# Kernel tuning notes

Hardware: AMD Instinct MI355X
Metric: run time of the kernel (lower is better)

The kernel has to match this reference:

```python
import jax, jax.numpy as jnp
import numpy as np

D_MODEL = 512
N_HEADS = 8
KV_OPTS = (8, 4, 1)
D_K = D_MODEL // N_HEADS


def setup_inputs() -> dict:
    key = jax.random.key(0)
    ks = jax.random.split(key, 32)
    it = iter(ks)
    s = 0.02
    inp = {"x": jax.random.normal(next(it), (64, 1024, D_MODEL), dtype=jnp.float32)}
    # router params
    inp["r_w1"] = jax.random.normal(next(it), (D_MODEL, D_MODEL // 4), jnp.float32) * s
    inp["r_b1"] = jnp.zeros((D_MODEL // 4,), jnp.float32)
    inp["r_w2"] = jax.random.normal(next(it), (D_MODEL // 4, len(KV_OPTS)), jnp.float32) * s
    inp["r_b2"] = jnp.zeros((len(KV_OPTS),), jnp.float32)
    # per-expert GQA params
    for i, nkv in enumerate(KV_OPTS):
        inp[f"wq{i}"] = jax.random.normal(next(it), (D_MODEL, D_MODEL), jnp.float32) * s
        inp[f"wk{i}"] = jax.random.normal(next(it), (D_MODEL, nkv * D_K), jnp.float32) * s
        inp[f"wv{i}"] = jax.random.normal(next(it), (D_MODEL, nkv * D_K), jnp.float32) * s
        inp[f"wo{i}"] = jax.random.normal(next(it), (D_MODEL, D_MODEL), jnp.float32) * s
    return inp


def gqa(x, wq, wk, wv, wo, n_kv):
    B, S, _ = x.shape
    groups = N_HEADS // n_kv
    q = (x @ wq).reshape(B, S, N_HEADS, D_K).transpose(0, 2, 1, 3)  # [B,H,S,Dk]
    k = (x @ wk).reshape(B, S, n_kv, D_K).transpose(0, 2, 1, 3)     # [B,Kv,S,Dk]
    v = (x @ wv).reshape(B, S, n_kv, D_K).transpose(0, 2, 1, 3)
    k = jnp.repeat(k, groups, axis=1)
    v = jnp.repeat(v, groups, axis=1)
    scores = jnp.einsum('bhqd,bhkd->bhqk', q, k) / jnp.sqrt(jnp.float32(D_K))
    attn = jax.nn.softmax(scores, axis=-1)
    out = jnp.einsum('bhqk,bhkd->bhqd', attn, v)
    out = out.transpose(0, 2, 1, 3).reshape(B, S, D_MODEL)
    return out @ wo


def reference(x, r_w1, r_b1, r_w2, r_b2,
              wq0, wk0, wv0, wo0,
              wq1, wk1, wv1, wo1,
              wq2, wk2, wv2, wo2):
    routing_input = x.mean(axis=1)                      # [B, D]
    logits = jax.nn.relu(routing_input @ r_w1 + r_b1) @ r_w2 + r_b2
    sel = jnp.argmax(jax.nn.softmax(logits, axis=-1), axis=-1)  # [B]

    params = [(wq0, wk0, wv0, wo0), (wq1, wk1, wv1, wo1), (wq2, wk2, wv2, wo2)]
    out = jnp.zeros_like(x)
    for i, nkv in enumerate(KV_OPTS):
        yi = gqa(x, *params[i], nkv)                    # [B,S,D]
        mask = (sel == i)[:, None, None]
        out = jnp.where(mask, yi, out)
    return out
```

## Files before the change

kernel.cpp:

```cpp
#include <hip/hip_runtime.h>
#include <hip/hip_bf16.h>

typedef __hip_bfloat16 bf16;
typedef __attribute__((ext_vector_type(8))) short short8;
typedef __attribute__((ext_vector_type(4))) float f32x4;
typedef __attribute__((ext_vector_type(16))) float f32x16;

#define MFMA_BF16(a,b,c) __builtin_amdgcn_mfma_f32_16x16x32_bf16(a,b,c,0,0,0)
#define MFMA32(a,b,c)    __builtin_amdgcn_mfma_f32_32x32x16_bf16(a,b,c,0,0,0)

#if __has_builtin(__builtin_amdgcn_exp2f)
#define EXPFN(x) __builtin_amdgcn_exp2f(x)
#define QSCALE 0.1803368801111204f
#else
#define EXPFN(x) __expf(x)
#define QSCALE 0.125f
#endif

__device__ __forceinline__ unsigned short bfbits(float f){
  bf16 h = __float2bfloat16(f);
  return __builtin_bit_cast(unsigned short, h);
}
__device__ __forceinline__ unsigned packbf(float a, float b){
  return (unsigned)bfbits(a) | ((unsigned)bfbits(b) << 16);
}

__device__ __forceinline__ void glds16(const void* g, void* l){
  __builtin_amdgcn_global_load_lds(
      (const __attribute__((address_space(1))) unsigned int*)(size_t)g,
      (__attribute__((address_space(3))) unsigned int*)l, 16, 0, 0);
}

__global__ __launch_bounds__(256)
void xconv_mean(const float* __restrict__ x, bf16* __restrict__ xb, float* __restrict__ part){
  int b = blockIdx.x, ch = blockIdx.y, t = threadIdx.x;
  size_t base = ((size_t)b*1024 + (size_t)ch*64)*512;
  const float2* xp = (const float2*)(x + base);
  unsigned* op = (unsigned*)(xb + base);
  float s0 = 0.f, s1 = 0.f;
#pragma unroll 4
  for (int s = 0; s < 64; ++s){
    float2 v = xp[s*256 + t];
    s0 += v.x; s1 += v.y;
    op[s*256 + t] = packbf(v.x, v.y);
  }
  float* pp = part + ((size_t)b*16 + ch)*512;
  pp[2*t]   = s0;
  pp[2*t+1] = s1;
}

__global__ void mean_final_kernel(const float* __restrict__ part, float* __restrict__ ri){
  int b = blockIdx.x;
  for (int dd = threadIdx.x; dd < 512; dd += 256){
    float a = 0.f;
    for (int c = 0; c < 16; ++c) a += part[((size_t)b*16 + c)*512 + dd];
    ri[(size_t)b*512 + dd] = a * (1.f/1024.f);
  }
}

__global__ __launch_bounds__(256)
void wconv(const float* __restrict__ w0, const float* __restrict__ w1, const float* __restrict__ w2,
           int N0, int N1, int N2, bf16* o0, bf16* o1, bf16* o2){
  int e = blockIdx.z;
  const float* W = e==0?w0:(e==1?w1:w2);
  int N = e==0?N0:(e==1?N1:N2);
  bf16* out = e==0?o0:(e==1?o1:o2);
  int n0 = blockIdx.y*64; if (n0 >= N) return;
  int k0 = blockIdx.x*64;
  __shared__ float tile[64][65];
  int t = threadIdx.x;
#pragma unroll
  for (int j=0;j<16;++j){
    int ee = j*256+t; int r = ee>>6, c = ee&63;
    tile[r][c] = W[(size_t)(k0+r)*N + n0+c];
  }
  __syncthreads();
#pragma unroll
  for (int j=0;j<16;++j){
    int ee = j*256+t; int n = ee>>6, kk = ee&63;
    out[(size_t)(n0+n)*512 + k0+kk] = __float2bfloat16(tile[kk][n]);
  }
}

__global__ void router_kernel(const float* __restrict__ ri,
                              const float* __restrict__ w1, const float* __restrict__ b1,
                              const float* __restrict__ w2, const float* __restrict__ b2,
                              int* __restrict__ sel){
  int b = blockIdx.x, t = threadIdx.x;
  __shared__ float h[128];
  __shared__ float lg[3];
  const float* rib = ri + (size_t)b*512;
  float acc = b1[t];
  for (int d = 0; d < 512; ++d) acc += rib[d]*w1[(size_t)d*128 + t];
  h[t] = fmaxf(acc, 0.f);
  __syncthreads();
  if (t < 3){
    float a = b2[t];
    for (int j = 0; j < 128; ++j) a += h[j]*w2[j*3 + t];
    lg[t] = a;
  }
  __syncthreads();
  if (t == 0){
    int best = 0; float bv = lg[0];
    if (lg[1] > bv){ bv = lg[1]; best = 1; }
    if (lg[2] > bv){ bv = lg[2]; best = 2; }
    sel[b] = best;
  }
}

template<int OUTMODE, int BN>
__global__ __launch_bounds__(256)
void gemm_mfma(const bf16* __restrict__ A,
               const bf16* __restrict__ Wt0, const bf16* __restrict__ Wt1, const bf16* __restrict__ Wt2,
               int N0, int N1, int N2,
               const int* __restrict__ sel, float oscale,
               void* __restrict__ outp){
  int b = blockIdx.z;
  int se = sel[b];
  const bf16* W = se==0?Wt0:(se==1?Wt1:Wt2);
  int N = se==0?N0:(se==1?N1:N2);
  int nb = blockIdx.y*BN;
  if (nb >= N) return;
  int mb = blockIdx.x*128;
  __shared__ __align__(16) bf16 As[128*64];
  __shared__ __align__(16) bf16 Bs[BN*64];
  int t = threadIdx.x, lane = t&63, w = t>>6, gg = lane>>4, cl = lane&15;
  f32x4 acc[2][BN/16] = {};
  const bf16* Ab = A + ((size_t)b*1024 + mb)*512;
  const bf16* Wb = W + (size_t)nb*512;

  for (int k0 = 0; k0 < 512; k0 += 64){
#pragma unroll
    for (int j=0;j<4;++j){
      int o = (j*256+t)*16;
      int r = o>>7;
      int gs = ((o>>4)&7) ^ (r&7);
      glds16(Ab + (size_t)r*512 + k0 + gs*8, (char*)As + o);
    }
#pragma unroll
    for (int j=0;j<BN/32;++j){
      int o = (j*256+t)*16;
      int r = o>>7;
      int gs = ((o>>4)&7) ^ (r&7);
      glds16(Wb + (size_t)r*512 + k0 + gs*8, (char*)Bs + o);
    }
    __syncthreads();

    short8 af[2][2];
#pragma unroll
    for (int mf=0;mf<2;++mf)
#pragma unroll
      for (int ks=0;ks<2;++ks){
        int r = w*32 + mf*16 + cl;
        int off = (ks*64 + gg*16) ^ ((r&7)<<4);
        af[mf][ks] = *(const short8*)((const char*)As + r*128 + off);
      }
#pragma unroll
    for (int nf=0;nf<BN/16;++nf){
      int r = nf*16 + cl;
      int rs = (r&7)<<4;
      short8 b0 = *(const short8*)((const char*)Bs + r*128 + ((0*64 + gg*16) ^ rs));
      short8 b1 = *(const short8*)((const char*)Bs + r*128 + ((1*64 + gg*16) ^ rs));
      acc[0][nf] = MFMA_BF16(af[0][0], b0, acc[0][nf]);
      acc[0][nf] = MFMA_BF16(af[0][1], b1, acc[0][nf]);
      acc[1][nf] = MFMA_BF16(af[1][0], b0, acc[1][nf]);
      acc[1][nf] = MFMA_BF16(af[1][1], b1, acc[1][nf]);
    }
    __syncthreads();
  }

#pragma unroll
  for (int mf=0;mf<2;++mf)
#pragma unroll
    for (int nf=0;nf<BN/16;++nf){
      int row = mb + w*32 + mf*16 + gg*4;
      int col = nb + nf*16 + cl;
      if (OUTMODE==0){
        bf16* C = (bf16*)outp;
#pragma unroll
        for (int i=0;i<4;++i)
          C[((size_t)b*1024 + row+i)*512 + col] = __float2bfloat16(acc[mf][nf][i]*oscale);
      } else if (OUTMODE==1){
        union { unsigned short u[4]; uint2 v; } pk;
#pragma unroll
        for (int i=0;i<4;++i) pk.u[i] = bfbits(acc[mf][nf][i]);
        *(uint2*)((bf16*)outp + ((size_t)b*512 + col)*1024 + row) = pk.v;
      } else {
        float* C = (float*)outp;
#pragma unroll
        for (int i=0;i<4;++i)
          C[((size_t)b*1024 + row+i)*512 + col] = acc[mf][nf][i];
      }
    }
}

__global__ __launch_bounds__(256, 4)
void attn_mfma(const bf16* __restrict__ Q, const bf16* __restrict__ K,
               const bf16* __restrict__ Vt, const int* __restrict__ sel,
               bf16* __restrict__ AO){
  int b = blockIdx.z, h = blockIdx.y, q0 = blockIdx.x*128;
  int se = sel[b];
  int nkv = se==0?8:(se==1?4:1);
  int kvh = h/(8/nkv);
  __shared__ __align__(16) bf16 Ks[2][64*64];
  __shared__ __align__(16) bf16 Vs[2][64*64];
  int t = threadIdx.x, l = t&63, w = t>>6, cl = l&31, hi = l>>5;
  const bf16* Kb = K + (size_t)b*1024*512 + (size_t)kvh*64;
  const bf16* Vb = Vt + ((size_t)b*512 + (size_t)kvh*64)*1024;
  const bf16* Qg = Q + ((size_t)b*1024 + q0 + w*32 + cl)*512 + h*64;

  short8 qf0 = *(const short8*)(Qg + hi*8);
  short8 qf1 = *(const short8*)(Qg + 16 + hi*8);
  short8 qf2 = *(const short8*)(Qg + 32 + hi*8);
  short8 qf3 = *(const short8*)(Qg + 48 + hi*8);

  f32x16 accO0 = {}, accO1 = {};
  float lrow = 0.f;
  int swz = (cl&7)<<4;

#define STAGE(CUR, S0) { \
  _Pragma("unroll") for (int j=0;j<2;++j){ \
    int o = (j*256+t)*16; int r = o>>7; int gs = ((o>>4)&7)^(r&7); \
    glds16(Kb + (size_t)((S0)+r)*512 + gs*8, (char*)Ks[CUR] + o); \
    glds16(Vb + (size_t)r*1024 + (S0) + gs*8, (char*)Vs[CUR] + o); \
  } }

  STAGE(0, 0)
  __syncthreads();
  int cur = 0;
  for (int kt=0; kt<16; ++kt){
    if (kt<15) STAGE(cur^1, (kt+1)*64)

    const char* Kt_ = (const char*)Ks[cur];
    const char* Vt_ = (const char*)Vs[cur];

    f32x16 sc0 = {}, sc1 = {};
    __builtin_amdgcn_s_setprio(1);
#pragma unroll
    for (int ks=0;ks<4;++ks){
      int off = (ks*32 + hi*16) ^ swz;
      short8 kf0 = *(const short8*)(Kt_ + (size_t)cl*128 + off);
      short8 kf1 = *(const short8*)(Kt_ + (size_t)(32+cl)*128 + off);
      short8 qq = ks==0?qf0:(ks==1?qf1:(ks==2?qf2:qf3));
      sc0 = MFMA32(kf0, qq, sc0);
      sc1 = MFMA32(kf1, qq, sc1);
    }
    __builtin_amdgcn_s_setprio(0);

    float ts0=0.f, ts1=0.f, ts2=0.f, ts3=0.f;
#pragma unroll
    for (int r=0;r<16;r+=2){
      float a0 = EXPFN(sc0[r]);   float a1 = EXPFN(sc0[r+1]);
      float a2 = EXPFN(sc1[r]);   float a3 = EXPFN(sc1[r+1]);
      sc0[r]=a0; sc0[r+1]=a1; sc1[r]=a2; sc1[r+1]=a3;
      ts0+=a0; ts1+=a1; ts2+=a2; ts3+=a3;
    }
    lrow += (ts0+ts1)+(ts2+ts3);

    unsigned pA0[4],pB0[4],pA1[4],pB1[4];
#pragma unroll
    for (int m=0;m<4;++m){
      pA0[m]=packbf(sc0[4*m+0],sc0[4*m+1]); pB0[m]=packbf(sc0[4*m+2],sc0[4*m+3]);
      pA1[m]=packbf(sc1[4*m+0],sc1[4*m+1]); pB1[m]=packbf(sc1[4*m+2],sc1[4*m+3]);
    }
    unsigned rA0[2],rB0[2],rA1[2],rB1[2];
#pragma unroll
    for (int f=0;f<2;++f){
      rA0[f] = __shfl_xor(hi ? pA0[2*f] : pA0[2*f+1], 32);
      rB0[f] = __shfl_xor(hi ? pB0[2*f] : pB0[2*f+1], 32);
      rA1[f] = __shfl_xor(hi ? pA1[2*f] : pA1[2*f+1], 32);
      rB1[f] = __shfl_xor(hi ? pB1[2*f] : pB1[2*f+1], 32);
    }
    short8 pF[4];
#pragma unroll
    for (int f=0;f<2;++f){
      uint4 u;
      u.x = hi ? rA0[f]     : pA0[2*f];
      u.y = hi ? rB0[f]     : pB0[2*f];
      u.z = hi ? pA0[2*f+1] : rA0[f];
      u.w = hi ? pB0[2*f+1] : rB0[f];
      pF[f] = __builtin_bit_cast(short8, u);
      uint4 v;
      v.x = hi ? rA1[f]     : pA1[2*f];
      v.y = hi ? rB1[f]     : pB1[2*f];
      v.z = hi ? pA1[2*f+1] : rA1[f];
      v.w = hi ? pB1[2*f+1] : rB1[f];
      pF[2+f] = __builtin_bit_cast(short8, v);
    }

    __builtin_amdgcn_s_setprio(1);
#pragma unroll
    for (int ks2=0;ks2<4;++ks2){
      int off = (ks2*32 + hi*16) ^ swz;
      short8 vf0 = *(const short8*)(Vt_ + (size_t)cl*128 + off);
      short8 vf1 = *(const short8*)(Vt_ + (size_t)(32+cl)*128 + off);
      accO0 = MFMA32(vf0, pF[ks2], accO0);
      accO1 = MFMA32(vf1, pF[ks2], accO1);
    }
    __builtin_amdgcn_s_setprio(0);
    __syncthreads();
    cur ^= 1;
  }
#undef STAGE

  float lfull = lrow + __shfl_xor(lrow, 32);
  float inv = 1.f/lfull;
  int row = q0 + w*32 + cl;
  bf16* Ao = AO + ((size_t)b*1024 + row)*512 + h*64;
#pragma unroll
  for (int u=0;u<4;++u){
    union{ unsigned short s[4]; uint2 v; } P0, P1;
#pragma unroll
    for (int j2=0;j2<4;++j2){
      P0.s[j2] = bfbits(accO0[4*u+j2]*inv);
      P1.s[j2] = bfbits(accO1[4*u+j2]*inv);
    }
    *(uint2*)(Ao + 8*u + 4*hi) = P0.v;
    *(uint2*)(Ao + 32 + 8*u + 4*hi) = P1.v;
  }
}

extern "C" void kernel_launch(void* const* d_in, const int* in_sizes, int n_in,
                              void* d_out, int out_size, void* d_ws, size_t ws_size,
                              hipStream_t stream){
  const float* x    = (const float*)d_in[0];
  const float* r_w1 = (const float*)d_in[1];
  const float* r_b1 = (const float*)d_in[2];
  const float* r_w2 = (const float*)d_in[3];
  const float* r_b2 = (const float*)d_in[4];
  const float* wq[3] = {(const float*)d_in[5], (const float*)d_in[9],  (const float*)d_in[13]};
  const float* wk[3] = {(const float*)d_in[6], (const float*)d_in[10], (const float*)d_in[14]};
  const float* wv[3] = {(const float*)d_in[7], (const float*)d_in[11], (const float*)d_in[15]};
  const float* wo[3] = {(const float*)d_in[8], (const float*)d_in[12], (const float*)d_in[16]};

  char* ws = (char*)d_ws;
  int*   sel      = (int*)ws;
  float* ri       = (float*)(ws + 4096);
  float* partials = (float*)(ws + 4096 + 131072);
  bf16*  Wtbuf    = (bf16*)(ws + 4096 + 131072 + 2097152);
  const size_t NE = (size_t)64*1024*512;
  bf16* xb = (bf16*)(ws + ((size_t)4<<20));
  bf16* Qb = xb + NE;
  bf16* Kb = Qb + NE;
  bf16* Vt = Kb + NE;
  bf16* AO = xb;

  xconv_mean<<<dim3(64,16), 256, 0, stream>>>(x, xb, partials);
  mean_final_kernel<<<64, 256, 0, stream>>>(partials, ri);
  router_kernel<<<64, 128, 0, stream>>>(ri, r_w1, r_b1, r_w2, r_b2, sel);

  {
    bf16 *o0 = Wtbuf, *o1 = o0 + (size_t)512*512, *o2 = o1 + (size_t)512*512;
    wconv<<<dim3(8,8,3), 256, 0, stream>>>(wq[0],wq[1],wq[2], 512,512,512, o0,o1,o2);
    gemm_mfma<0,128><<<dim3(8,4,64), 256, 0, stream>>>(xb, o0,o1,o2, 512,512,512, sel, (float)QSCALE, Qb);
  }
  {
    bf16 *o0 = Wtbuf, *o1 = o0 + (size_t)512*512, *o2 = o1 + (size_t)256*512;
    wconv<<<dim3(8,8,3), 256, 0, stream>>>(wk[0],wk[1],wk[2], 512,256,64, o0,o1,o2);
    gemm_mfma<0,64><<<dim3(8,8,64), 256, 0, stream>>>(xb, o0,o1,o2, 512,256,64, sel, 1.0f, Kb);
  }
  {
    bf16 *o0 = Wtbuf, *o1 = o0 + (size_t)512*512, *o2 = o1 + (size_t)256*512;
    wconv<<<dim3(8,8,3), 256, 0, stream>>>(wv[0],wv[1],wv[2], 512,256,64, o0,o1,o2);
    gemm_mfma<1,64><<<dim3(8,8,64), 256, 0, stream>>>(xb, o0,o1,o2, 512,256,64, sel, 1.0f, Vt);
  }

  attn_mfma<<<dim3(8,8,64), 256, 0, stream>>>(Qb, Kb, Vt, sel, AO);

  {
    bf16 *o0 = Wtbuf, *o1 = o0 + (size_t)512*512, *o2 = o1 + (size_t)512*512;
    wconv<<<dim3(8,8,3), 256, 0, stream>>>(wo[0],wo[1],wo[2], 512,512,512, o0,o1,o2);
    gemm_mfma<2,128><<<dim3(8,4,64), 256, 0, stream>>>(AO, o0,o1,o2, 512,512,512, sel, 1.0f, (float*)d_out);
  }
}
```

Measured before the change: 441.2 us.

## Fuse router stages, batch weight conversions, and merge K/V projection GEMMs

```diff
diff --git a/kernel.cpp b/kernel.cpp
--- a/kernel.cpp
+++ b/kernel.cpp
@@ -9,13 +9,11 @@
 #define MFMA_BF16(a,b,c) __builtin_amdgcn_mfma_f32_16x16x32_bf16(a,b,c,0,0,0)
 #define MFMA32(a,b,c)    __builtin_amdgcn_mfma_f32_32x32x16_bf16(a,b,c,0,0,0)
 
-#if __has_builtin(__builtin_amdgcn_exp2f)
-#define EXPFN(x) __builtin_amdgcn_exp2f(x)
+__device__ __forceinline__ float exp2_hw(float x){
+  float r; asm("v_exp_f32 %0, %1" : "=v"(r) : "v"(x)); return r;
+}
+#define EXPFN(x) exp2_hw(x)
 #define QSCALE 0.1803368801111204f
-#else
-#define EXPFN(x) __expf(x)
-#define QSCALE 0.125f
-#endif
 
 __device__ __forceinline__ unsigned short bfbits(float f){
   bf16 h = __float2bfloat16(f);
@@ -49,50 +47,26 @@
   pp[2*t+1] = s1;
 }
 
-__global__ void mean_final_kernel(const float* __restrict__ part, float* __restrict__ ri){
-  int b = blockIdx.x;
-  for (int dd = threadIdx.x; dd < 512; dd += 256){
+__global__ __launch_bounds__(256)
+void router_fused(const float* __restrict__ part,
+                  const float* __restrict__ w1, const float* __restrict__ b1,
+                  const float* __restrict__ w2, const float* __restrict__ b2,
+                  int* __restrict__ sel){
+  int b = blockIdx.x, t = threadIdx.x;
+  __shared__ float rs[512];
+  __shared__ float h[128];
+  __shared__ float lg[3];
+  for (int dd = t; dd < 512; dd += 256){
     float a = 0.f;
     for (int c = 0; c < 16; ++c) a += part[((size_t)b*16 + c)*512 + dd];
-    ri[(size_t)b*512 + dd] = a * (1.f/1024.f);
-  }
-}
-
-__global__ __launch_bounds__(256)
-void wconv(const float* __restrict__ w0, const float* __restrict__ w1, const float* __restrict__ w2,
-           int N0, int N1, int N2, bf16* o0, bf16* o1, bf16* o2){
-  int e = blockIdx.z;
-  const float* W = e==0?w0:(e==1?w1:w2);
-  int N = e==0?N0:(e==1?N1:N2);
-  bf16* out = e==0?o0:(e==1?o1:o2);
-  int n0 = blockIdx.y*64; if (n0 >= N) return;
-  int k0 = blockIdx.x*64;
-  __shared__ float tile[64][65];
-  int t = threadIdx.x;
-#pragma unroll
-  for (int j=0;j<16;++j){
-    int ee = j*256+t; int r = ee>>6, c = ee&63;
-    tile[r][c] = W[(size_t)(k0+r)*N + n0+c];
+    rs[dd] = a * (1.f/1024.f);
   }
   __syncthreads();
-#pragma unroll
-  for (int j=0;j<16;++j){
-    int ee = j*256+t; int n = ee>>6, kk = ee&63;
-    out[(size_t)(n0+n)*512 + k0+kk] = __float2bfloat16(tile[kk][n]);
-  }
-}
-
-__global__ void router_kernel(const float* __restrict__ ri,
-                              const float* __restrict__ w1, const float* __restrict__ b1,
-                              const float* __restrict__ w2, const float* __restrict__ b2,
-                              int* __restrict__ sel){
-  int b = blockIdx.x, t = threadIdx.x;
-  __shared__ float h[128];
-  __shared__ float lg[3];
-  const float* rib = ri + (size_t)b*512;
-  float acc = b1[t];
-  for (int d = 0; d < 512; ++d) acc += rib[d]*w1[(size_t)d*128 + t];
-  h[t] = fmaxf(acc, 0.f);
+  if (t < 128){
+    float acc = b1[t];
+    for (int d = 0; d < 512; ++d) acc += rs[d]*w1[(size_t)d*128 + t];
+    h[t] = fmaxf(acc, 0.f);
+  }
   __syncthreads();
   if (t < 3){
     float a = b2[t];
@@ -106,6 +80,46 @@
     if (lg[2] > bv){ bv = lg[2]; best = 2; }
     sel[b] = best;
   }
+}
+
+__device__ __forceinline__ void wconv_tile(const float* __restrict__ W, int N,
+                                           bf16* __restrict__ dst, int n0, int k0){
+  __shared__ float tile[64][65];
+  int t = threadIdx.x;
+#pragma unroll
+  for (int j=0;j<16;++j){
+    int ee = j*256+t; int r = ee>>6, c = ee&63;
+    tile[r][c] = W[(size_t)(k0+r)*N + n0+c];
+  }
+  __syncthreads();
+#pragma unroll
+  for (int j=0;j<16;++j){
+    int ee = j*256+t; int n = ee>>6, kk = ee&63;
+    dst[(size_t)(n0+n)*512 + k0+kk] = __float2bfloat16(tile[kk][n]);
+  }
+}
+
+__global__ __launch_bounds__(256)
+void wconv_qkv(const float* q0,const float* q1,const float* q2,
+               const float* k0p,const float* k1p,const float* k2p,
+               const float* v0p,const float* v1p,const float* v2p,
+               bf16* wqt, bf16* wkt, bf16* wvt){
+  int zz = blockIdx.z;
+  const float* W; int N; bf16* dst;
+  if (zz < 3){ W = zz==0?q0:(zz==1?q1:q2); N = 512; dst = wqt + (size_t)zz*512*512; }
+  else if (zz < 6){ int e=zz-3; W = e==0?k0p:(e==1?k1p:k2p); N = e==0?512:(e==1?256:64);
+                    dst = wkt + (size_t)(e==0?0:(e==1?512:768))*512; }
+  else { int e=zz-6; W = e==0?v0p:(e==1?v1p:v2p); N = e==0?512:(e==1?256:64);
+         dst = wvt + (size_t)(e==0?0:(e==1?512:768))*512; }
+  int n0 = blockIdx.y*64; if (n0 >= N) return;
+  wconv_tile(W, N, dst, n0, blockIdx.x*64);
+}
+
+__global__ __launch_bounds__(256)
+void wconv_o(const float* o0,const float* o1,const float* o2, bf16* wot){
+  int e = blockIdx.z;
+  const float* W = e==0?o0:(e==1?o1:o2);
+  wconv_tile(W, 512, wot + (size_t)e*512*512, blockIdx.y*64, blockIdx.x*64);
 }
 
 template<int OUTMODE, int BN>
@@ -159,8 +173,8 @@
     for (int nf=0;nf<BN/16;++nf){
       int r = nf*16 + cl;
       int rs = (r&7)<<4;
-      short8 b0 = *(const short8*)((const char*)Bs + r*128 + ((0*64 + gg*16) ^ rs));
-      short8 b1 = *(const short8*)((const char*)Bs + r*128 + ((1*64 + gg*16) ^ rs));
+      short8 b0 = *(const short8*)((const char*)Bs + r*128 + ((gg*16) ^ rs));
+      short8 b1 = *(const short8*)((const char*)Bs + r*128 + ((64 + gg*16) ^ rs));
       acc[0][nf] = MFMA_BF16(af[0][0], b0, acc[0][nf]);
       acc[0][nf] = MFMA_BF16(af[0][1], b1, acc[0][nf]);
       acc[1][nf] = MFMA_BF16(af[1][0], b0, acc[1][nf]);
@@ -180,17 +194,96 @@
 #pragma unroll
         for (int i=0;i<4;++i)
           C[((size_t)b*1024 + row+i)*512 + col] = __float2bfloat16(acc[mf][nf][i]*oscale);
-      } else if (OUTMODE==1){
-        union { unsigned short u[4]; uint2 v; } pk;
-#pragma unroll
-        for (int i=0;i<4;++i) pk.u[i] = bfbits(acc[mf][nf][i]);
-        *(uint2*)((bf16*)outp + ((size_t)b*512 + col)*1024 + row) = pk.v;
       } else {
         float* C = (float*)outp;
 #pragma unroll
         for (int i=0;i<4;++i)
           C[((size_t)b*1024 + row+i)*512 + col] = acc[mf][nf][i];
       }
+    }
+}
+
+__global__ __launch_bounds__(256)
+void gemm_kv(const bf16* __restrict__ A,
+             const bf16* __restrict__ wkt, const bf16* __restrict__ wvt,
+             const int* __restrict__ sel,
+             bf16* __restrict__ Kb, bf16* __restrict__ Vt){
+  int b = blockIdx.z;
+  int se = sel[b];
+  int NK = se==0?512:(se==1?256:64);
+  int nb = blockIdx.y*64;
+  if (nb >= NK) return;
+  int roff = se==0?0:(se==1?512:768);
+  int mb = blockIdx.x*128;
+  __shared__ __align__(16) bf16 As[128*64];
+  __shared__ __align__(16) bf16 Bk[64*64];
+  __shared__ __align__(16) bf16 Bv[64*64];
+  int t = threadIdx.x, lane = t&63, w = t>>6, gg = lane>>4, cl = lane&15;
+  f32x4 accK[2][4] = {}, accV[2][4] = {};
+  const bf16* Ab = A + ((size_t)b*1024 + mb)*512;
+  const bf16* Wk = wkt + (size_t)(roff+nb)*512;
+  const bf16* Wv = wvt + (size_t)(roff+nb)*512;
+
+  for (int k0 = 0; k0 < 512; k0 += 64){
+#pragma unroll
+    for (int j=0;j<4;++j){
+      int o = (j*256+t)*16;
+      int r = o>>7;
+      int gs = ((o>>4)&7) ^ (r&7);
+      glds16(Ab + (size_t)r*512 + k0 + gs*8, (char*)As + o);
+    }
+#pragma unroll
+    for (int j=0;j<2;++j){
+      int o = (j*256+t)*16;
+      int r = o>>7;
+      int gs = ((o>>4)&7) ^ (r&7);
+      glds16(Wk + (size_t)r*512 + k0 + gs*8, (char*)Bk + o);
+      glds16(Wv + (size_t)r*512 + k0 + gs*8, (char*)Bv + o);
+    }
+    __syncthreads();
+
+    short8 af[2][2];
+#pragma unroll
+    for (int mf=0;mf<2;++mf)
+#pragma unroll
+      for (int ks=0;ks<2;++ks){
+        int r = w*32 + mf*16 + cl;
+        int off = (ks*64 + gg*16) ^ ((r&7)<<4);
+        af[mf][ks] = *(const short8*)((const char*)As + r*128 + off);
+      }
+#pragma unroll
+    for (int nf=0;nf<4;++nf){
+      int r = nf*16 + cl;
+      int rs = (r&7)<<4;
+      short8 bk0 = *(const short8*)((const char*)Bk + r*128 + ((gg*16) ^ rs));
+      short8 bk1 = *(const short8*)((const char*)Bk + r*128 + ((64 + gg*16) ^ rs));
+      short8 bv0 = *(const short8*)((const char*)Bv + r*128 + ((gg*16) ^ rs));
+      short8 bv1 = *(const short8*)((const char*)Bv + r*128 + ((64 + gg*16) ^ rs));
+      accK[0][nf] = MFMA_BF16(af[0][0], bk0, accK[0][nf]);
+      accK[0][nf] = MFMA_BF16(af[0][1], bk1, accK[0][nf]);
+      accK[1][nf] = MFMA_BF16(af[1][0], bk0, accK[1][nf]);
+      accK[1][nf] = MFMA_BF16(af[1][1], bk1, accK[1][nf]);
+      accV[0][nf] = MFMA_BF16(af[0][0], bv0, accV[0][nf]);
+      accV[0][nf] = MFMA_BF16(af[0][1], bv1, accV[0][nf]);
+      accV[1][nf] = MFMA_BF16(af[1][0], bv0, accV[1][nf]);
+      accV[1][nf] = MFMA_BF16(af[1][1], bv1, accV[1][nf]);
+    }
+    __syncthreads();
+  }
+
+#pragma unroll
+  for (int mf=0;mf<2;++mf)
+#pragma unroll
+    for (int nf=0;nf<4;++nf){
+      int row = mb + w*32 + mf*16 + gg*4;
+      int col = nb + nf*16 + cl;
+#pragma unroll
+      for (int i=0;i<4;++i)
+        Kb[((size_t)b*1024 + row+i)*512 + col] = __float2bfloat16(accK[mf][nf][i]);
+      union { unsigned short u[4]; uint2 v; } pk;
+#pragma unroll
+      for (int i=0;i<4;++i) pk.u[i] = bfbits(accV[mf][nf][i]);
+      *(uint2*)(Vt + ((size_t)b*512 + col)*1024 + row) = pk.v;
     }
 }
 
@@ -335,9 +428,11 @@
 
   char* ws = (char*)d_ws;
   int*   sel      = (int*)ws;
-  float* ri       = (float*)(ws + 4096);
-  float* partials = (float*)(ws + 4096 + 131072);
-  bf16*  Wtbuf    = (bf16*)(ws + 4096 + 131072 + 2097152);
+  float* partials = (float*)(ws + 4096);
+  bf16*  wqt      = (bf16*)(ws + 4096);
+  bf16*  wkt      = (bf16*)(ws + 4096 + 1572864);
+  bf16*  wvt      = (bf16*)(ws + 4096 + 1572864 + 851968);
+  bf16*  wot      = wqt;
   const size_t NE = (size_t)64*1024*512;
   bf16* xb = (bf16*)(ws + ((size_t)4<<20));
   bf16* Qb = xb + NE;
@@ -346,30 +441,22 @@
   bf16* AO = xb;
 
   xconv_mean<<<dim3(64,16), 256, 0, stream>>>(x, xb, partials);
-  mean_final_kernel<<<64, 256, 0, stream>>>(partials, ri);
-  router_kernel<<<64, 128, 0, stream>>>(ri, r_w1, r_b1, r_w2, r_b2, sel);
-
-  {
-    bf16 *o0 = Wtbuf, *o1 = o0 + (size_t)512*512, *o2 = o1 + (size_t)512*512;
-    wconv<<<dim3(8,8,3), 256, 0, stream>>>(wq[0],wq[1],wq[2], 512,512,512, o0,o1,o2);
-    gemm_mfma<0,128><<<dim3(8,4,64), 256, 0, stream>>>(xb, o0,o1,o2, 512,512,512, sel, (float)QSCALE, Qb);
-  }
-  {
-    bf16 *o0 = Wtbuf, *o1 = o0 + (size_t)512*512, *o2 = o1 + (size_t)256*512;
-    wconv<<<dim3(8,8,3), 256, 0, stream>>>(wk[0],wk[1],wk[2], 512,256,64, o0,o1,o2);
-    gemm_mfma<0,64><<<dim3(8,8,64), 256, 0, stream>>>(xb, o0,o1,o2, 512,256,64, sel, 1.0f, Kb);
-  }
-  {
-    bf16 *o0 = Wtbuf, *o1 = o0 + (size_t)512*512, *o2 = o1 + (size_t)256*512;
-    wconv<<<dim3(8,8,3), 256, 0, stream>>>(wv[0],wv[1],wv[2], 512,256,64, o0,o1,o2);
-    gemm_mfma<1,64><<<dim3(8,8,64), 256, 0, stream>>>(xb, o0,o1,o2, 512,256,64, sel, 1.0f, Vt);
-  }
+  router_fused<<<64, 256, 0, stream>>>(partials, r_w1, r_b1, r_w2, r_b2, sel);
+
+  wconv_qkv<<<dim3(8,8,9), 256, 0, stream>>>(wq[0],wq[1],wq[2], wk[0],wk[1],wk[2],
+                                             wv[0],wv[1],wv[2], wqt, wkt, wvt);
+
+  gemm_mfma<0,128><<<dim3(8,4,64), 256, 0, stream>>>(
+      xb, wqt, wqt + (size_t)512*512, wqt + (size_t)2*512*512,
+      512,512,512, sel, (float)QSCALE, Qb);
+
+  gemm_kv<<<dim3(8,8,64), 256, 0, stream>>>(xb, wkt, wvt, sel, Kb, Vt);
+
+  wconv_o<<<dim3(8,8,3), 256, 0, stream>>>(wo[0],wo[1],wo[2], wot);
 
   attn_mfma<<<dim3(8,8,64), 256, 0, stream>>>(Qb, Kb, Vt, sel, AO);
 
-  {
-    bf16 *o0 = Wtbuf, *o1 = o0 + (size_t)512*512, *o2 = o1 + (size_t)512*512;
-    wconv<<<dim3(8,8,3), 256, 0, stream>>>(wo[0],wo[1],wo[2], 512,512,512, o0,o1,o2);
-    gemm_mfma<2,128><<<dim3(8,4,64), 256, 0, stream>>>(AO, o0,o1,o2, 512,512,512, sel, 1.0f, (float*)d_out);
-  }
-}
+  gemm_mfma<2,128><<<dim3(8,4,64), 256, 0, stream>>>(
+      AO, wot, wot + (size_t)512*512, wot + (size_t)2*512*512,
+      512,512,512, sel, 1.0f, (float*)d_out);
+}
```

Measured after the change: 414.0 us. -6.2%, faster.
